# Performance work log

Measured on AMD Instinct MI355X. Metric: run time of the kernel, lower is better.

The kernel has to match this reference:

```python
import jax, jax.numpy as jnp
import numpy as np

B, S, D = 2, 2048, 2048
H, DK, DV, L = 16, 128, 128, 64


def setup_inputs() -> dict:
    key = jax.random.key(0)
    ks = jax.random.split(key, 12)
    s = lambda k, shape, fan_in: jax.random.normal(k, shape, jnp.float32) / np.sqrt(fan_in)
    return {
        "queries": jax.random.normal(ks[0], (B, S, D), jnp.float32),
        "keys": jax.random.normal(ks[1], (B, S, D), jnp.float32),
        "values": jax.random.normal(ks[2], (B, S, D), jnp.float32),
        "Wq": s(ks[3], (D, H * DK), D), "bq": jnp.zeros((H * DK,), jnp.float32),
        "Wlk": s(ks[4], (D, H * L), D), "blk": jnp.zeros((H * L,), jnp.float32),
        "Wlv": s(ks[5], (D, H * L), D), "blv": jnp.zeros((H * L,), jnp.float32),
        "Wkr": s(ks[6], (L, DK), L),
        "Wvr": s(ks[7], (L, DV), L),
        "Wout": s(ks[8], (H * DV, D), H * DV), "bout": jnp.zeros((D,), jnp.float32),
    }


def reference(queries, keys, values, Wq, bq, Wlk, blk, Wlv, blv, Wkr, Wvr, Wout, bout):
    b, sq, _ = queries.shape
    sk = keys.shape[1]
    # projections -> [b, h, s, d]
    q = (queries @ Wq + bq).reshape(b, sq, H, DK).transpose(0, 2, 1, 3)
    lk = (keys @ Wlk + blk).reshape(b, sk, H, L).transpose(0, 2, 1, 3)
    lv = (values @ Wlv + blv).reshape(b, sk, H, L).transpose(0, 2, 1, 3)
    k = lk @ Wkr  # [b,h,sk,DK] latent -> key reconstruction
    v = lv @ Wvr  # [b,h,sk,DV]
    scores = jnp.einsum('bhqd,bhkd->bhqk', q, k) / np.sqrt(DK).astype(np.float32)
    causal = jnp.triu(jnp.ones((sq, sk), dtype=bool), k=1)
    scores = jnp.where(causal, -jnp.inf, scores)
    attn = jax.nn.softmax(scores, axis=-1)
    out = jnp.einsum('bhqk,bhkd->bhqd', attn, v)
    out = out.transpose(0, 2, 1, 3).reshape(b, sq, H * DV)
    return out @ Wout + bout
```

## Files before the change

### kernel.cpp

```cpp
#include <hip/hip_runtime.h>
#include <cstdint>
#include <cstddef>

typedef _Float16 f16;
typedef __attribute__((ext_vector_type(8))) _Float16 f16x8;
typedef __attribute__((ext_vector_type(4))) _Float16 f16x4;
typedef __attribute__((ext_vector_type(4))) float f32x4;

constexpr int kB  = 2;
constexpr int kS  = 2048;
constexpr int kD  = 2048;
constexpr int kH  = 16;
constexpr int kL  = 64;
constexpr int kHL = kH * kL;
constexpr int kBS = kB * kS;

__device__ __forceinline__ void load_lds16(const void* g, void* l) {
  __builtin_amdgcn_global_load_lds((const __attribute__((address_space(1))) void*)g,
                                   (__attribute__((address_space(3))) void*)l, 16, 0, 0);
}

__device__ __forceinline__ f32x4 mfma16(f16x8 a, f16x8 b, f32x4 c) {
  return __builtin_amdgcn_mfma_f32_16x16x32_f16(a, b, c, 0, 0, 0);
}

__global__ void cast4(const float* __restrict__ a, const float* __restrict__ b,
                      const float* __restrict__ c, const float* __restrict__ d,
                      f16* __restrict__ oa, f16* __restrict__ ob,
                      f16* __restrict__ oc, f16* __restrict__ od) {
  const int z = blockIdx.z;
  int i = blockIdx.x * 256 + threadIdx.x;
  if (z == 3 && i >= kD * kD / 4) return;
  const float* in = z == 0 ? a : z == 1 ? b : z == 2 ? c : d;
  f16* out = z == 0 ? oa : z == 1 ? ob : z == 2 ? oc : od;
  float4 f = ((const float4*)in)[i];
  f16x4 o; o[0] = (f16)f.x; o[1] = (f16)f.y; o[2] = (f16)f.z; o[3] = (f16)f.w;
  ((f16x4*)out)[i] = o;
}

__device__ __forceinline__ void transpose_body(const float* __restrict__ in,
                                               f16* __restrict__ out, int R, int C) {
  const int r0 = blockIdx.y * 64, c0 = blockIdx.x * 64;
  __shared__ float tile[64][65];
  const int t = threadIdx.x;
  const int cc = t & 63, rr = t >> 6;
#pragma unroll
  for (int p = 0; p < 16; p++) {
    int r = p * 4 + rr;
    tile[r][cc] = in[(size_t)(r0 + r) * C + c0 + cc];
  }
  __syncthreads();
#pragma unroll
  for (int p = 0; p < 16; p++) {
    int c = p * 4 + rr;
    out[(size_t)(c0 + c) * R + r0 + cc] = (f16)tile[cc][c];
  }
}

__global__ __launch_bounds__(256) void transpose3(const float* __restrict__ Wlk,
                                                  const float* __restrict__ Wlv,
                                                  const float* __restrict__ Wout,
                                                  f16* __restrict__ Wlkt,
                                                  f16* __restrict__ Wlvt,
                                                  f16* __restrict__ WoutT) {
  const int z = blockIdx.z;
  if (z < 2 && blockIdx.x >= 16) return;
  if (z == 0) transpose_body(Wlk, Wlkt, 2048, 1024);
  else if (z == 1) transpose_body(Wlv, Wlvt, 2048, 1024);
  else transpose_body(Wout, WoutT, 2048, 2048);
}

__global__ void fold_bq(const float* __restrict__ bq, const float* __restrict__ Wkr,
                        float* __restrict__ bql) {
  int hl = blockIdx.x * 256 + threadIdx.x;
  if (hl >= kHL) return;
  int h = hl >> 6, l = hl & 63;
  float s = 0.f;
  for (int c = 0; c < 128; c++) s += bq[h * 128 + c] * Wkr[l * 128 + c];
  bql[hl] = s;
}

__global__ __launch_bounds__(256) void fold2(const float* __restrict__ Wkr,
                                             const float* __restrict__ Wvr,
                                             const f16* __restrict__ Wq16,
                                             const f16* __restrict__ WoutT,
                                             f16* __restrict__ Wqlt,
                                             f16* __restrict__ W2t) {
  __shared__ f16 sA[64 * 136];
  __shared__ f16 sB[128 * 128];
  const int z = blockIdx.z;
  const int h = blockIdx.y;
  const int d0 = blockIdx.x * 128;
  const float* Wsm = z ? Wvr : Wkr;
  const f16* Bsrc = (z ? WoutT : Wq16) + h * 128;
  const int tid = threadIdx.x;
  const int w = tid >> 6, lane = tid & 63;
  const int quad = lane >> 4, l16 = lane & 15;

#pragma unroll
  for (int it = 0; it < 8; it++) {
    int i = it * 256 + tid;
    float4 f = ((const float4*)Wsm)[i];
    int e = i * 4, r = e >> 7, c = e & 127;
    f16x4 o; o[0] = (f16)f.x; o[1] = (f16)f.y; o[2] = (f16)f.z; o[3] = (f16)f.w;
    *(f16x4*)&sA[r * 136 + c] = o;
  }
#pragma unroll
  for (int c = 0; c < 8; c++) {
    int rbase = w * 32 + c * 4;
    load_lds16(Bsrc + (size_t)(d0 + rbase + (lane >> 4)) * 2048 + (lane & 15) * 8,
               &sB[rbase * 128]);
  }
  __syncthreads();

  if (z == 0) {
    f32x4 acc[4][2];
    for (int mt = 0; mt < 4; mt++)
      for (int nt = 0; nt < 2; nt++) acc[mt][nt] = (f32x4){0.f, 0.f, 0.f, 0.f};
#pragma unroll
    for (int ks = 0; ks < 4; ks++) {
      f16x8 af[4], bf[2];
#pragma unroll
      for (int mt = 0; mt < 4; mt++)
        af[mt] = *(const f16x8*)&sA[(mt * 16 + l16) * 136 + ks * 32 + quad * 8];
#pragma unroll
      for (int nt = 0; nt < 2; nt++)
        bf[nt] = *(const f16x8*)&sB[(w * 32 + nt * 16 + l16) * 128 + ks * 32 + quad * 8];
#pragma unroll
      for (int mt = 0; mt < 4; mt++)
#pragma unroll
        for (int nt = 0; nt < 2; nt++) acc[mt][nt] = mfma16(af[mt], bf[nt], acc[mt][nt]);
    }
#pragma unroll
    for (int mt = 0; mt < 4; mt++)
#pragma unroll
      for (int nt = 0; nt < 2; nt++)
#pragma unroll
        for (int r = 0; r < 4; r++) {
          int row = mt * 16 + quad * 4 + r;
          int col = d0 + w * 32 + nt * 16 + l16;
          Wqlt[(size_t)(h * 64 + row) * 2048 + col] = (f16)acc[mt][nt][r];
        }
  } else {
    f32x4 acc[2][4];
    for (int mt = 0; mt < 2; mt++)
      for (int nt = 0; nt < 4; nt++) acc[mt][nt] = (f32x4){0.f, 0.f, 0.f, 0.f};
#pragma unroll
    for (int ks = 0; ks < 4; ks++) {
      f16x8 af[2], bf[4];
#pragma unroll
      for (int mt = 0; mt < 2; mt++)
        af[mt] = *(const f16x8*)&sB[(w * 32 + mt * 16 + l16) * 128 + ks * 32 + quad * 8];
#pragma unroll
      for (int nt = 0; nt < 4; nt++)
        bf[nt] = *(const f16x8*)&sA[(nt * 16 + l16) * 136 + ks * 32 + quad * 8];
#pragma unroll
      for (int mt = 0; mt < 2; mt++)
#pragma unroll
        for (int nt = 0; nt < 4; nt++) acc[mt][nt] = mfma16(af[mt], bf[nt], acc[mt][nt]);
    }
#pragma unroll
    for (int mt = 0; mt < 2; mt++)
#pragma unroll
      for (int nt = 0; nt < 4; nt++)
#pragma unroll
        for (int r = 0; r < 4; r++) {
          int row = d0 + w * 32 + mt * 16 + quad * 4 + r;
          int col = nt * 16 + l16;
          W2t[(size_t)row * 1024 + h * 64 + col] = (f16)acc[mt][nt][r];
        }
  }
}

template <typename OutT, bool HAS_BIAS>
__device__ __forceinline__ void gemm_body(const f16* __restrict__ A, const f16* __restrict__ Bt,
                                          const float* __restrict__ bias, OutT* __restrict__ C,
                                          int N, int K, int m0, int n0) {
  __shared__ f16 sAall[3 * 128 * 32];
  __shared__ f16 sBall[3 * 128 * 32];
  const int tid = threadIdx.x;
  const int w = tid >> 6, lane = tid & 63;
  const int quad = lane >> 4, l16 = lane & 15;
  const int wm = w >> 1, wn = w & 1;

  const int srow = lane >> 2;
  const int schunk = (lane & 3) ^ ((lane >> 3) & 3);
  const f16* aptr = A + (size_t)(m0 + w * 32 + srow) * K + schunk * 8;
  const f16* bptr = Bt + (size_t)(n0 + w * 32 + srow) * K + schunk * 8;
  const int g0 = w * 1024;
  const int g1 = g0 + 512;

  const int xoff = (quad ^ ((l16 >> 1) & 3)) * 8;

  f32x4 acc[4][4];
  for (int i = 0; i < 4; i++)
    for (int j = 0; j < 4; j++) acc[i][j] = (f32x4){0.f, 0.f, 0.f, 0.f};

  auto stage = [&](int buf, int k0) {
    f16* dA = &sAall[buf * 4096];
    f16* dB = &sBall[buf * 4096];
    load_lds16(aptr + k0, dA + g0);
    load_lds16(aptr + (size_t)16 * K + k0, dA + g1);
    load_lds16(bptr + k0, dB + g0);
    load_lds16(bptr + (size_t)16 * K + k0, dB + g1);
  };

  const int nt = K >> 5;
  stage(0, 0);
  stage(1, 32);
  asm volatile("s_waitcnt vmcnt(4)" ::: "memory");
  __builtin_amdgcn_sched_barrier(0);
  __builtin_amdgcn_s_barrier();
  __builtin_amdgcn_sched_barrier(0);

  int bc = 0, bs = 2;
  for (int t = 0; t < nt; ++t) {
    if (t + 2 < nt) stage(bs, (t + 2) * 32);
    const f16* sAc = &sAall[bc * 4096];
    const f16* sBc = &sBall[bc * 4096];
    f16x8 af[4], bfr[4];
#pragma unroll
    for (int mt = 0; mt < 4; mt++)
      af[mt] = *(const f16x8*)&sAc[(wm * 64 + mt * 16 + l16) * 32 + xoff];
#pragma unroll
    for (int nf = 0; nf < 4; nf++)
      bfr[nf] = *(const f16x8*)&sBc[(wn * 64 + nf * 16 + l16) * 32 + xoff];
#pragma unroll
    for (int mt = 0; mt < 4; mt++) {
#pragma unroll
      for (int nf = 0; nf < 4; nf++)
        acc[mt][nf] = mfma16(af[mt], bfr[nf], acc[mt][nf]);
    }
    if (t + 1 < nt) {
      if (t + 2 < nt)
        asm volatile("s_waitcnt vmcnt(4)" ::: "memory");
      else
        asm volatile("s_waitcnt vmcnt(0)" ::: "memory");
      __builtin_amdgcn_sched_barrier(0);
      __builtin_amdgcn_s_barrier();
      __builtin_amdgcn_sched_barrier(0);
    }
    bc = bc == 2 ? 0 : bc + 1;
    bs = bs == 2 ? 0 : bs + 1;
  }

#pragma unroll
  for (int mt = 0; mt < 4; mt++) {
#pragma unroll
    for (int nf = 0; nf < 4; nf++) {
      int col = n0 + wn * 64 + nf * 16 + l16;
      float bv = HAS_BIAS ? bias[col] : 0.f;
#pragma unroll
      for (int r = 0; r < 4; r++) {
        int row = m0 + wm * 64 + mt * 16 + quad * 4 + r;
        C[(size_t)row * N + col] = (OutT)(acc[mt][nf][r] + bv);
      }
    }
  }
}

__device__ __forceinline__ int xcd_swizzle(int flat, int nwg) {
  const int cpx = nwg >> 3;
  return (flat & 7) * cpx + (flat >> 3);
}

__global__ __launch_bounds__(256) void gemm3_f16(
    const f16* __restrict__ A0, const f16* __restrict__ A1, const f16* __restrict__ A2,
    const f16* __restrict__ B0, const f16* __restrict__ B1, const f16* __restrict__ B2,
    const float* __restrict__ c0, const float* __restrict__ c1, const float* __restrict__ c2,
    f16* __restrict__ C0, f16* __restrict__ C1, f16* __restrict__ C2, int N, int K) {
  const f16* A = blockIdx.z == 0 ? A0 : blockIdx.z == 1 ? A1 : A2;
  const f16* Bt = blockIdx.z == 0 ? B0 : blockIdx.z == 1 ? B1 : B2;
  const float* bias = blockIdx.z == 0 ? c0 : blockIdx.z == 1 ? c1 : c2;
  f16* C = blockIdx.z == 0 ? C0 : blockIdx.z == 1 ? C1 : C2;
  const int nx = gridDim.x;
  int swz = xcd_swizzle(blockIdx.y * nx + blockIdx.x, nx * gridDim.y);
  gemm_body<f16, true>(A, Bt, bias, C, N, K, (swz / nx) * 128, (swz % nx) * 128);
}

__global__ __launch_bounds__(256) void gemm_f32(const f16* __restrict__ A,
                                                const f16* __restrict__ Bt,
                                                const float* __restrict__ bias,
                                                float* __restrict__ C, int N, int K) {
  const int nx = gridDim.x;
  int swz = xcd_swizzle(blockIdx.y * nx + blockIdx.x, nx * gridDim.y);
  gemm_body<float, true>(A, Bt, bias, C, N, K, (swz / nx) * 128, (swz % nx) * 128);
}

__global__ __launch_bounds__(256) void transpose_lv(const f16* __restrict__ LV,
                                                    f16* __restrict__ LVt) {
  const int bh = blockIdx.y, b = bh >> 4, h = bh & 15;
  const int s0 = blockIdx.x * 64;
  __shared__ f16 tile[64][65];
  const int t = threadIdx.x;
  const int c0 = t & 63, r0 = t >> 6;
#pragma unroll
  for (int r = 0; r < 16; r++) {
    int s = r * 4 + r0;
    tile[s][c0] = LV[(size_t)(b * kS + s0 + s) * kHL + h * kL + c0];
  }
  __syncthreads();
#pragma unroll
  for (int r = 0; r < 16; r++) {
    int vl = r * 4 + r0;
    LVt[((size_t)bh * kL + vl) * kS + s0 + c0] = tile[c0][vl];
  }
}

__global__ __launch_bounds__(256) void attn(const f16* __restrict__ Qlat,
                                            const f16* __restrict__ LK,
                                            const f16* __restrict__ LVt,
                                            f16* __restrict__ Ctx) {
  const int bh = blockIdx.y, b = bh >> 4, h = bh & 15;
  const int pair = blockIdx.x;
  const int tid = threadIdx.x;
  const int w = tid >> 6, lane = tid & 63;
  const int quad = lane >> 4, l16 = lane & 15;

  __shared__ f16 sK[2][64 * 64];
  __shared__ f16 sV[2][64 * 64];
  __shared__ f16 sP[4][16 * 72];

  const f16* qbase = Qlat + (size_t)b * kS * kHL + h * kL;
  const f16* kbase = LK + (size_t)b * kS * kHL + h * kL;
  const f16* vbase = LVt + (size_t)bh * kL * kS;

  const float cscale = 0.08838834764831845f * 1.4426950408889634f;
  const int rowA = lane >> 3;
  const int colSw = (((lane & 7) ^ (lane >> 3)) << 3);
  const int sw0 = ((quad ^ (l16 & 7)) << 3);
  const int sw1 = (((4 + quad) ^ (l16 & 7)) << 3);

  for (int which = 0; which < 2; which++) {
    const int t = which ? (31 - pair) : pair;
    const int q0 = t * 64;
    const int qrow = q0 + w * 16 + l16;
    const int qg = qrow;
    const int ntile = t + 1;

    f16x8 aq[2];
#pragma unroll
    for (int ks = 0; ks < 2; ks++)
      aq[ks] = *(const f16x8*)(qbase + (size_t)qrow * kHL + ks * 32 + quad * 8);

    f32x4 acc[4];
    for (int nt = 0; nt < 4; nt++) acc[nt] = (f32x4){0.f, 0.f, 0.f, 0.f};
    float m_s = -3.0e38f;
    float l_part = 0.f;

    __syncthreads();
    {
      const int rl = w * 16;
      load_lds16(kbase + (size_t)(rl + rowA) * kHL + colSw, &sK[0][rl * 64]);
      load_lds16(vbase + (size_t)(rl + rowA) * kS + colSw, &sV[0][rl * 64]);
      load_lds16(kbase + (size_t)(rl + 8 + rowA) * kHL + colSw, &sK[0][(rl + 8) * 64]);
      load_lds16(vbase + (size_t)(rl + 8 + rowA) * kS + colSw, &sV[0][(rl + 8) * 64]);
    }
    int cur = 0;

    for (int it = 0; it < ntile; ++it) {
      const int kv0 = it * 64;
      __syncthreads();

      if (it + 1 < ntile) {
        const int nkv = kv0 + 64;
        f16* dK = &sK[cur ^ 1][0];
        f16* dV = &sV[cur ^ 1][0];
        const int rl = w * 16;
        load_lds16(kbase + (size_t)(nkv + rl + rowA) * kHL + colSw, dK + rl * 64);
        load_lds16(vbase + (size_t)(rl + rowA) * kS + nkv + colSw, dV + rl * 64);
        load_lds16(kbase + (size_t)(nkv + rl + 8 + rowA) * kHL + colSw, dK + (rl + 8) * 64);
        load_lds16(vbase + (size_t)(rl + 8 + rowA) * kS + nkv + colSw, dV + (rl + 8) * 64);
      }
      const f16* sKc = &sK[cur][0];
      const f16* sVc = &sV[cur][0];

      f32x4 sc[4];
      for (int nt = 0; nt < 4; nt++) sc[nt] = (f32x4){0.f, 0.f, 0.f, 0.f};
#pragma unroll
      for (int ks = 0; ks < 2; ks++) {
        const int sw = ks ? sw1 : sw0;
        f16x8 bk[4];
#pragma unroll
        for (int nt = 0; nt < 4; nt++)
          bk[nt] = *(const f16x8*)&sKc[(nt * 16 + l16) * 64 + sw];
#pragma unroll
        for (int nt = 0; nt < 4; nt++) sc[nt] = mfma16(bk[nt], aq[ks], sc[nt]);
      }

      if (kv0 == q0) {
#pragma unroll
        for (int nt = 0; nt < 4; nt++) {
#pragma unroll
          for (int r = 0; r < 4; r++) {
            int kvg = kv0 + nt * 16 + quad * 4 + r;
            if (kvg > qg) sc[nt][r] = -1.0e30f;
          }
        }
      }

      float tm = -3.0e38f;
#pragma unroll
      for (int nt = 0; nt < 4; nt++)
        tm = fmaxf(tm, fmaxf(fmaxf(sc[nt][0], sc[nt][1]), fmaxf(sc[nt][2], sc[nt][3])));
      tm = fmaxf(tm, __shfl_xor(tm, 16));
      tm = fmaxf(tm, __shfl_xor(tm, 32));
      const float tms = tm * cscale;

      if (!__all(tms <= m_s)) {
        const float mnew = fmaxf(m_s, tms);
        const float alpha = __builtin_amdgcn_exp2f(m_s - mnew);
        m_s = mnew;
        l_part *= alpha;
        float ar[4];
#pragma unroll
        for (int r = 0; r < 4; r++) ar[r] = __shfl(alpha, quad * 4 + r);
#pragma unroll
        for (int nt = 0; nt < 4; nt++)
#pragma unroll
          for (int r = 0; r < 4; r++) acc[nt][r] *= ar[r];
      }

      float ps = 0.f;
#pragma unroll
      for (int nt = 0; nt < 4; nt++) {
        f16x4 pk;
#pragma unroll
        for (int r = 0; r < 4; r++) {
          float p = __builtin_amdgcn_exp2f(__builtin_fmaf(sc[nt][r], cscale, -m_s));
          ps += p;
          pk[r] = (f16)p;
        }
        *(f16x4*)&sP[w][l16 * 72 + nt * 16 + quad * 4] = pk;
      }
      l_part += ps;

#pragma unroll
      for (int ks = 0; ks < 2; ks++) {
        const int sw = ks ? sw1 : sw0;
        f16x8 ap = *(const f16x8*)&sP[w][l16 * 72 + ks * 32 + quad * 8];
        f16x8 bv[4];
#pragma unroll
        for (int nt = 0; nt < 4; nt++)
          bv[nt] = *(const f16x8*)&sVc[(nt * 16 + l16) * 64 + sw];
#pragma unroll
        for (int nt = 0; nt < 4; nt++) acc[nt] = mfma16(ap, bv[nt], acc[nt]);
      }
      cur ^= 1;
    }

    float lfull = l_part;
    lfull += __shfl_xor(lfull, 16);
    lfull += __shfl_xor(lfull, 32);
    float inv[4];
#pragma unroll
    for (int r = 0; r < 4; r++) inv[r] = 1.f / __shfl(lfull, quad * 4 + r);
#pragma unroll
    for (int r = 0; r < 4; r++) {
      int qout = q0 + w * 16 + quad * 4 + r;
      size_t base = (size_t)(b * kS + qout) * kHL + h * kL;
#pragma unroll
      for (int nt = 0; nt < 4; nt++)
        Ctx[base + nt * 16 + l16] = (f16)(acc[nt][r] * inv[r]);
    }
  }
}

extern "C" void kernel_launch(void* const* d_in, const int* in_sizes, int n_in,
                              void* d_out, int out_size, void* d_ws, size_t ws_size,
                              hipStream_t stream) {
  (void)in_sizes; (void)n_in; (void)out_size; (void)ws_size;
  const float* queries = (const float*)d_in[0];
  const float* keys    = (const float*)d_in[1];
  const float* values  = (const float*)d_in[2];
  const float* Wq      = (const float*)d_in[3];
  const float* bq      = (const float*)d_in[4];
  const float* Wlk     = (const float*)d_in[5];
  const float* blk     = (const float*)d_in[6];
  const float* Wlv     = (const float*)d_in[7];
  const float* blv     = (const float*)d_in[8];
  const float* Wkr     = (const float*)d_in[9];
  const float* Wvr     = (const float*)d_in[10];
  const float* Wout    = (const float*)d_in[11];
  const float* bout    = (const float*)d_in[12];

  char* ws = (char*)d_ws;
  size_t off = 0;
  auto alloc = [&](size_t bytes) {
    void* p = ws + off;
    off += (bytes + 255) & ~(size_t)255;
    return p;
  };
  f16* qb    = (f16*)alloc((size_t)kBS * kD * 2);
  f16* kb    = (f16*)alloc((size_t)kBS * kD * 2);
  f16* vb    = (f16*)alloc((size_t)kBS * kD * 2);
  f16* Wqlt  = (f16*)alloc((size_t)kHL * kD * 2);
  f16* Wlkt  = (f16*)alloc((size_t)kHL * kD * 2);
  f16* Wlvt  = (f16*)alloc((size_t)kHL * kD * 2);
  f16* W2t   = (f16*)alloc((size_t)kD * kHL * 2);
  float* bql = (float*)alloc(kHL * 4);
  f16* Qlat  = (f16*)alloc((size_t)kBS * kHL * 2);
  f16* LKb   = (f16*)alloc((size_t)kBS * kHL * 2);
  f16* LVb   = (f16*)alloc((size_t)kBS * kHL * 2);
  f16* Wq16  = Qlat;
  f16* WoutT = LKb;
  f16* LVtb = qb;
  f16* Ctx  = kb;

  const int n4 = kBS * kD / 4;
  cast4<<<dim3(n4 / 256, 1, 4), 256, 0, stream>>>(queries, keys, values, Wq, qb, kb, vb, Wq16);
  transpose3<<<dim3(32, 32, 3), 256, 0, stream>>>(Wlk, Wlv, Wout, Wlkt, Wlvt, WoutT);
  fold_bq<<<kHL / 256, 256, 0, stream>>>(bq, Wkr, bql);
  fold2<<<dim3(16, 16, 2), 256, 0, stream>>>(Wkr, Wvr, Wq16, WoutT, Wqlt, W2t);

  gemm3_f16<<<dim3(kHL / 128, kBS / 128, 3), 256, 0, stream>>>(
      qb, kb, vb, Wqlt, Wlkt, Wlvt, bql, blk, blv, Qlat, LKb, LVb, kHL, kD);

  transpose_lv<<<dim3(kS / 64, kB * kH), 256, 0, stream>>>(LVb, LVtb);
  attn<<<dim3(16, kB * kH), 256, 0, stream>>>(Qlat, LKb, LVtb, Ctx);
  gemm_f32<<<dim3(kD / 128, kBS / 128), 256, 0, stream>>>(Ctx, W2t, bout, (float*)d_out, kD, kHL);
}
```

Before: 357.2 us.

## Restructure GEMMs as 8-wave 256x128 tiles with phased load/MFMA interleave

Replaces the 4-wave 128x128 GEMM body with an 8-wave kernel that computes 256x128 tiles over 64-wide K steps, using 3-stage LDS buffering. Each K step is split into four phases, and each phase interleaves part of the next tile's global-to-LDS loads with one MFMA burst raised to high priority via s_setprio. The aim is to raise arithmetic intensity per tile and overlap memory traffic with MFMA work. The attention kernel also gets setprio around its MFMA loops. The cost is much larger LDS use (~144KB), more barriers per iteration, and fewer workgroups in the grid.

```diff
diff --git a/kernel.cpp b/kernel.cpp
--- a/kernel.cpp
+++ b/kernel.cpp
@@ -173,87 +173,120 @@
 }
 
 template <typename OutT, bool HAS_BIAS>
-__device__ __forceinline__ void gemm_body(const f16* __restrict__ A, const f16* __restrict__ Bt,
-                                          const float* __restrict__ bias, OutT* __restrict__ C,
-                                          int N, int K, int m0, int n0) {
-  __shared__ f16 sAall[3 * 128 * 32];
-  __shared__ f16 sBall[3 * 128 * 32];
+__device__ __forceinline__ void gemm8p_body(const f16* __restrict__ A, const f16* __restrict__ Bt,
+                                            const float* __restrict__ bias, OutT* __restrict__ C,
+                                            int N, int K, int m0, int n0) {
+  __shared__ f16 sA[3 * 256 * 64];
+  __shared__ f16 sB[3 * 128 * 64];
   const int tid = threadIdx.x;
   const int w = tid >> 6, lane = tid & 63;
   const int quad = lane >> 4, l16 = lane & 15;
-  const int wm = w >> 1, wn = w & 1;
-
-  const int srow = lane >> 2;
-  const int schunk = (lane & 3) ^ ((lane >> 3) & 3);
-  const f16* aptr = A + (size_t)(m0 + w * 32 + srow) * K + schunk * 8;
-  const f16* bptr = Bt + (size_t)(n0 + w * 32 + srow) * K + schunk * 8;
-  const int g0 = w * 1024;
-  const int g1 = g0 + 512;
-
-  const int xoff = (quad ^ ((l16 >> 1) & 3)) * 8;
-
-  f32x4 acc[4][4];
-  for (int i = 0; i < 4; i++)
-    for (int j = 0; j < 4; j++) acc[i][j] = (f32x4){0.f, 0.f, 0.f, 0.f};
-
-  auto stage = [&](int buf, int k0) {
-    f16* dA = &sAall[buf * 4096];
-    f16* dB = &sBall[buf * 4096];
-    load_lds16(aptr + k0, dA + g0);
-    load_lds16(aptr + (size_t)16 * K + k0, dA + g1);
-    load_lds16(bptr + k0, dB + g0);
-    load_lds16(bptr + (size_t)16 * K + k0, dB + g1);
-  };
-
-  const int nt = K >> 5;
-  stage(0, 0);
-  stage(1, 32);
-  asm volatile("s_waitcnt vmcnt(4)" ::: "memory");
+  const int wm = w >> 2, wn = w & 3;
+  const int sw0 = ((quad ^ (l16 & 7)) << 3);
+  const int sw1 = (((4 + quad) ^ (l16 & 7)) << 3);
+
+  const int srow = lane >> 3;
+  const int schunk = (lane & 7) ^ srow;
+  const f16* aG = A + (size_t)(m0 + w * 8 + srow) * K + schunk * 8;
+  const f16* bG = Bt + (size_t)(n0 + w * 8 + srow) * K + schunk * 8;
+  const int ldsOff = (w * 8) * 64 + lane * 8;
+
+  f32x4 acc[8][2];
+#pragma unroll
+  for (int i = 0; i < 8; i++) {
+    acc[i][0] = (f32x4){0.f, 0.f, 0.f, 0.f};
+    acc[i][1] = (f32x4){0.f, 0.f, 0.f, 0.f};
+  }
+
+#define STAGE_A(b, k0, j) load_lds16(aG + (size_t)((j) * 64) * K + (k0), \
+                                     &sA[(b) * 16384 + (j) * 4096 + ldsOff])
+#define STAGE_B(b, k0, j) load_lds16(bG + (size_t)((j) * 64) * K + (k0), \
+                                     &sB[(b) * 8192 + (j) * 4096 + ldsOff])
+#define PHASE_PRE()  do { __builtin_amdgcn_sched_barrier(0); __builtin_amdgcn_s_barrier(); \
+    asm volatile("s_waitcnt lgkmcnt(0)" ::: "memory"); __builtin_amdgcn_sched_barrier(0); \
+    __builtin_amdgcn_s_setprio(1); } while (0)
+#define PHASE_POST() do { __builtin_amdgcn_s_setprio(0); __builtin_amdgcn_sched_barrier(0); \
+    __builtin_amdgcn_s_barrier(); } while (0)
+
+  const int nt = K >> 6;
+#pragma unroll
+  for (int j = 0; j < 4; j++) STAGE_A(0, 0, j);
+  STAGE_B(0, 0, 0); STAGE_B(0, 0, 1);
+#pragma unroll
+  for (int j = 0; j < 4; j++) STAGE_A(1, 64, j);
+  STAGE_B(1, 64, 0); STAGE_B(1, 64, 1);
+  asm volatile("s_waitcnt vmcnt(6)" ::: "memory");
   __builtin_amdgcn_sched_barrier(0);
   __builtin_amdgcn_s_barrier();
   __builtin_amdgcn_sched_barrier(0);
 
   int bc = 0, bs = 2;
   for (int t = 0; t < nt; ++t) {
-    if (t + 2 < nt) stage(bs, (t + 2) * 32);
-    const f16* sAc = &sAall[bc * 4096];
-    const f16* sBc = &sBall[bc * 4096];
-    f16x8 af[4], bfr[4];
-#pragma unroll
-    for (int mt = 0; mt < 4; mt++)
-      af[mt] = *(const f16x8*)&sAc[(wm * 64 + mt * 16 + l16) * 32 + xoff];
-#pragma unroll
-    for (int nf = 0; nf < 4; nf++)
-      bfr[nf] = *(const f16x8*)&sBc[(wn * 64 + nf * 16 + l16) * 32 + xoff];
-#pragma unroll
-    for (int mt = 0; mt < 4; mt++) {
-#pragma unroll
-      for (int nf = 0; nf < 4; nf++)
-        acc[mt][nf] = mfma16(af[mt], bfr[nf], acc[mt][nf]);
-    }
+    const f16* a = &sA[bc * 16384];
+    const f16* b = &sB[bc * 8192];
+    const bool st = (t + 2) < nt;
+    const int kS = (t + 2) << 6;
+    f16x8 af[8], bf;
+
+#pragma unroll
+    for (int mt = 0; mt < 8; mt++)
+      af[mt] = *(const f16x8*)&a[(wm * 128 + mt * 16 + l16) * 64 + sw0];
+    bf = *(const f16x8*)&b[(wn * 32 + l16) * 64 + sw0];
+    if (st) { STAGE_A(bs, kS, 0); STAGE_A(bs, kS, 1); }
+    PHASE_PRE();
+#pragma unroll
+    for (int mt = 0; mt < 8; mt++) acc[mt][0] = mfma16(af[mt], bf, acc[mt][0]);
+    PHASE_POST();
+
+    bf = *(const f16x8*)&b[(wn * 32 + 16 + l16) * 64 + sw0];
+    if (st) { STAGE_A(bs, kS, 2); STAGE_A(bs, kS, 3); }
+    PHASE_PRE();
+#pragma unroll
+    for (int mt = 0; mt < 8; mt++) acc[mt][1] = mfma16(af[mt], bf, acc[mt][1]);
+    PHASE_POST();
+
+#pragma unroll
+    for (int mt = 0; mt < 8; mt++)
+      af[mt] = *(const f16x8*)&a[(wm * 128 + mt * 16 + l16) * 64 + sw1];
+    bf = *(const f16x8*)&b[(wn * 32 + l16) * 64 + sw1];
+    if (st) STAGE_B(bs, kS, 0);
+    PHASE_PRE();
+#pragma unroll
+    for (int mt = 0; mt < 8; mt++) acc[mt][0] = mfma16(af[mt], bf, acc[mt][0]);
+    PHASE_POST();
+
+    bf = *(const f16x8*)&b[(wn * 32 + 16 + l16) * 64 + sw1];
+    if (st) STAGE_B(bs, kS, 1);
+    PHASE_PRE();
+#pragma unroll
+    for (int mt = 0; mt < 8; mt++) acc[mt][1] = mfma16(af[mt], bf, acc[mt][1]);
+    __builtin_amdgcn_s_setprio(0);
     if (t + 1 < nt) {
-      if (t + 2 < nt)
-        asm volatile("s_waitcnt vmcnt(4)" ::: "memory");
-      else
-        asm volatile("s_waitcnt vmcnt(0)" ::: "memory");
-      __builtin_amdgcn_sched_barrier(0);
-      __builtin_amdgcn_s_barrier();
-      __builtin_amdgcn_sched_barrier(0);
-    }
+      if (st) asm volatile("s_waitcnt vmcnt(6)" ::: "memory");
+      else    asm volatile("s_waitcnt vmcnt(0)" ::: "memory");
+    }
+    __builtin_amdgcn_sched_barrier(0);
+    __builtin_amdgcn_s_barrier();
+    __builtin_amdgcn_sched_barrier(0);
+
     bc = bc == 2 ? 0 : bc + 1;
     bs = bs == 2 ? 0 : bs + 1;
   }
-
-#pragma unroll
-  for (int mt = 0; mt < 4; mt++) {
-#pragma unroll
-    for (int nf = 0; nf < 4; nf++) {
-      int col = n0 + wn * 64 + nf * 16 + l16;
+#undef STAGE_A
+#undef STAGE_B
+#undef PHASE_PRE
+#undef PHASE_POST
+
+#pragma unroll
+  for (int mt = 0; mt < 8; mt++) {
+#pragma unroll
+    for (int nh = 0; nh < 2; nh++) {
+      int col = n0 + wn * 32 + nh * 16 + l16;
       float bv = HAS_BIAS ? bias[col] : 0.f;
 #pragma unroll
       for (int r = 0; r < 4; r++) {
-        int row = m0 + wm * 64 + mt * 16 + quad * 4 + r;
-        C[(size_t)row * N + col] = (OutT)(acc[mt][nf][r] + bv);
+        int row = m0 + wm * 128 + mt * 16 + quad * 4 + r;
+        C[(size_t)row * N + col] = (OutT)(acc[mt][nh][r] + bv);
       }
     }
   }
@@ -264,7 +297,7 @@
   return (flat & 7) * cpx + (flat >> 3);
 }
 
-__global__ __launch_bounds__(256) void gemm3_f16(
+__global__ __launch_bounds__(512) void gemm3_f16(
     const f16* __restrict__ A0, const f16* __restrict__ A1, const f16* __restrict__ A2,
     const f16* __restrict__ B0, const f16* __restrict__ B1, const f16* __restrict__ B2,
     const float* __restrict__ c0, const float* __restrict__ c1, const float* __restrict__ c2,
@@ -275,16 +308,16 @@
   f16* C = blockIdx.z == 0 ? C0 : blockIdx.z == 1 ? C1 : C2;
   const int nx = gridDim.x;
   int swz = xcd_swizzle(blockIdx.y * nx + blockIdx.x, nx * gridDim.y);
-  gemm_body<f16, true>(A, Bt, bias, C, N, K, (swz / nx) * 128, (swz % nx) * 128);
-}
-
-__global__ __launch_bounds__(256) void gemm_f32(const f16* __restrict__ A,
+  gemm8p_body<f16, true>(A, Bt, bias, C, N, K, (swz / nx) * 256, (swz % nx) * 128);
+}
+
+__global__ __launch_bounds__(512) void gemm_f32(const f16* __restrict__ A,
                                                 const f16* __restrict__ Bt,
                                                 const float* __restrict__ bias,
                                                 float* __restrict__ C, int N, int K) {
   const int nx = gridDim.x;
   int swz = xcd_swizzle(blockIdx.y * nx + blockIdx.x, nx * gridDim.y);
-  gemm_body<float, true>(A, Bt, bias, C, N, K, (swz / nx) * 128, (swz % nx) * 128);
+  gemm8p_body<float, true>(A, Bt, bias, C, N, K, (swz / nx) * 256, (swz % nx) * 128);
 }
 
 __global__ __launch_bounds__(256) void transpose_lv(const f16* __restrict__ LV,
@@ -384,8 +417,10 @@
 #pragma unroll
         for (int nt = 0; nt < 4; nt++)
           bk[nt] = *(const f16x8*)&sKc[(nt * 16 + l16) * 64 + sw];
+        __builtin_amdgcn_s_setprio(1);
 #pragma unroll
         for (int nt = 0; nt < 4; nt++) sc[nt] = mfma16(bk[nt], aq[ks], sc[nt]);
+        __builtin_amdgcn_s_setprio(0);
       }
 
       if (kv0 == q0) {
@@ -443,8 +478,10 @@
 #pragma unroll
         for (int nt = 0; nt < 4; nt++)
           bv[nt] = *(const f16x8*)&sVc[(nt * 16 + l16) * 64 + sw];
+        __builtin_amdgcn_s_setprio(1);
 #pragma unroll
         for (int nt = 0; nt < 4; nt++) acc[nt] = mfma16(ap, bv[nt], acc[nt]);
+        __builtin_amdgcn_s_setprio(0);
       }
       cur ^= 1;
     }
@@ -513,10 +550,10 @@
   fold_bq<<<kHL / 256, 256, 0, stream>>>(bq, Wkr, bql);
   fold2<<<dim3(16, 16, 2), 256, 0, stream>>>(Wkr, Wvr, Wq16, WoutT, Wqlt, W2t);
 
-  gemm3_f16<<<dim3(kHL / 128, kBS / 128, 3), 256, 0, stream>>>(
+  gemm3_f16<<<dim3(kHL / 128, kBS / 256, 3), 512, 0, stream>>>(
       qb, kb, vb, Wqlt, Wlkt, Wlvt, bql, blk, blv, Qlat, LKb, LVb, kHL, kD);
 
   transpose_lv<<<dim3(kS / 64, kB * kH), 256, 0, stream>>>(LVb, LVtb);
   attn<<<dim3(16, kB * kH), 256, 0, stream>>>(Qlat, LKb, LVtb, Ctx);
-  gemm_f32<<<dim3(kD / 128, kBS / 128), 256, 0, stream>>>(Ctx, W2t, bout, (float*)d_out, kD, kHL);
-}
+  gemm_f32<<<dim3(kD / 128, kBS / 256), 512, 0, stream>>>(Ctx, W2t, bout, (float*)d_out, kD, kHL);
+}
```

Result: slower. 395.6 us (+10.7%).
